# Kernel optimization log

Measured on AMD Instinct MI355X. Metric: run time of the kernel, lower is better.

## Reference

```python
import jax, jax.numpy as jnp
import numpy as np

B, N, E = 2, 20000, 320000
ND, ED, HD, L = 64, 32, 256, 4


def setup_inputs() -> dict:
    key = jax.random.key(0)
    ks = jax.random.split(key, 16)
    w = lambda k, shape: jax.random.normal(k, shape, jnp.float32) / np.sqrt(shape[-2])
    return {
        "node_features": jax.random.normal(ks[0], (B, N, ND), jnp.float32),
        "edge_indices": jax.random.randint(ks[1], (B, E, 2), 0, N, jnp.int64),
        "edge_features": jax.random.normal(ks[2], (B, E, ED), jnp.float32),
        "in_W": w(ks[3], (ND, HD)),
        "in_b": jnp.zeros((HD,), jnp.float32),
        "mW1": w(ks[4], (L, 2 * HD + ED, HD)),
        "mb1": jnp.zeros((L, HD), jnp.float32),
        "mW2": w(ks[5], (L, HD, HD)),
        "mb2": jnp.zeros((L, HD), jnp.float32),
        "uW1": w(ks[6], (L, HD + HD, HD)),
        "ub1": jnp.zeros((L, HD), jnp.float32),
        "uW2": w(ks[7], (L, HD, HD)),
        "ub2": jnp.zeros((L, HD), jnp.float32),
        "out_W": w(ks[8], (HD, ND)),
        "out_b": jnp.zeros((ND,), jnp.float32),
    }


def _mp_layer(h, edge_indices, edge_features, W1, b1, W2, b2, V1, c1, V2, c2):
    """One message passing layer, vmapped over batch of graphs."""
    def per_graph(nodes, edges, efeat):
        src = nodes[edges[:, 0]]                      # [E, HD] gather
        dst = nodes[edges[:, 1]]                      # [E, HD] gather
        msg_in = jnp.concatenate([src, dst, efeat], axis=-1)  # [E, 2HD+ED]
        msg = jax.nn.gelu(msg_in @ W1 + b1) @ W2 + b2          # [E, HD]
        agg = jnp.zeros((nodes.shape[0], W2.shape[1]), nodes.dtype)
        agg = agg.at[edges[:, 1]].add(msg)                     # scatter-add [N, HD]
        upd_in = jnp.concatenate([nodes, agg], axis=-1)        # [N, 2HD]
        return jax.nn.gelu(upd_in @ V1 + c1) @ V2 + c2         # [N, HD]

    return jax.vmap(per_graph)(h, edge_indices, edge_features)


def reference(node_features, edge_indices, edge_features, in_W, in_b,
              mW1, mb1, mW2, mb2, uW1, ub1, uW2, ub2, out_W, out_b):
    h = node_features @ in_W + in_b                  # [B, N, HD]
    num_layers = mW1.shape[0]
    for l in range(num_layers):
        h_new = _mp_layer(h, edge_indices, edge_features,
                          mW1[l], mb1[l], mW2[l], mb2[l],
                          uW1[l], ub1[l], uW2[l], ub2[l])
        h = h + h_new                                # residual
    return h @ out_W + out_b                         # [B, N, ND]
```

## Files before the change

### kernel.cpp

```cpp
#include <hip/hip_runtime.h>

#define NN 20000
#define NE 320000
#define NB 2
#define HDIM 256
#define NDIM 64
#define EDIM 32
#define NL 4
#define CHUNK 16

typedef short short8 __attribute__((ext_vector_type(8)));
typedef float f32x4 __attribute__((ext_vector_type(4)));

__device__ __forceinline__ float gelu_af(float x) {
    float x3 = x * x * x;
    float e = exp2f(2.3022082f * fmaf(0.044715f, x3, x));
    return fmaf(-x, __builtin_amdgcn_rcpf(e + 1.0f), x);
}

__device__ __forceinline__ unsigned short f2bf(float f) {
    unsigned int x = __float_as_uint(f);
    unsigned int r = (x + 0x7fffu + ((x >> 16) & 1u)) >> 16;
    return (unsigned short)r;
}
__device__ __forceinline__ float bf2f(unsigned short h) {
    return __uint_as_float(((unsigned int)h) << 16);
}

__global__ __launch_bounds__(256) void tr_k(
    const float* __restrict__ inW, const float* __restrict__ mW1,
    const float* __restrict__ mW2, const float* __restrict__ uW1,
    const float* __restrict__ uW2, const float* __restrict__ outW,
    unsigned short* __restrict__ dst)
{
    const int id = blockIdx.z;
    const float* src; int K, N; size_t doff;
    if (id == 0)       { src = inW;  K = 64;  N = 256; doff = 0; }
    else if (id <= 4)  { int l = id - 1;  src = mW1 + (size_t)l * 544 * 256; K = 544; N = 256; doff = 16384   + (size_t)l * 139264; }
    else if (id <= 8)  { int l = id - 5;  src = mW2 + (size_t)l * 256 * 256; K = 256; N = 256; doff = 573440  + (size_t)l * 65536;  }
    else if (id <= 12) { int l = id - 9;  src = uW1 + (size_t)l * 512 * 256; K = 512; N = 256; doff = 835584  + (size_t)l * 131072; }
    else if (id <= 16) { int l = id - 13; src = uW2 + (size_t)l * 256 * 256; K = 256; N = 256; doff = 1359872 + (size_t)l * 65536;  }
    else               { src = outW; K = 256; N = 64;  doff = 1622016; }

    const int k0 = blockIdx.x * 32, n0 = blockIdx.y * 32;
    if (k0 >= K || n0 >= N) return;

    __shared__ float tile[32][33];
    const int tx = threadIdx.x & 31, ty = threadIdx.x >> 5;
    #pragma unroll
    for (int i = 0; i < 4; ++i) {
        int k = k0 + ty + i * 8, n = n0 + tx;
        tile[ty + i * 8][tx] = (k < K && n < N) ? src[(size_t)k * N + n] : 0.f;
    }
    __syncthreads();
    #pragma unroll
    for (int i = 0; i < 4; ++i) {
        int n = n0 + ty + i * 8, k = k0 + tx;
        if (n < N && k < K) dst[doff + (size_t)n * K + k] = f2bf(tile[tx][ty + i * 8]);
    }
}

__global__ __launch_bounds__(256) void wv_k(
    const float* __restrict__ mW2, const float* __restrict__ uW1,
    unsigned short* __restrict__ w2v1bT)
{
    const int l = blockIdx.z;
    const float* W2  = mW2 + (size_t)l * 65536;
    const float* V1b = uW1 + (size_t)l * 131072 + 65536;
    const int n0 = blockIdx.x * 16, k0 = blockIdx.y * 16;
    const int tx = threadIdx.x & 15, ty = threadIdx.x >> 4;
    __shared__ float sW[16][17], sV[16][17];
    float acc = 0.f;
    for (int j0 = 0; j0 < 256; j0 += 16) {
        sW[ty][tx] = W2[(size_t)(k0 + ty) * 256 + j0 + tx];
        sV[ty][tx] = V1b[(size_t)(j0 + ty) * 256 + n0 + tx];
        __syncthreads();
        #pragma unroll
        for (int jj = 0; jj < 16; ++jj)
            acc = fmaf(sW[ty][jj], sV[jj][tx], acc);
        __syncthreads();
    }
    w2v1bT[(size_t)l * 65536 + (size_t)(n0 + tx) * 256 + (k0 + ty)] = f2bf(acc);
}

__global__ void bv_k(const float* __restrict__ mb1, const float* __restrict__ mb2,
                     const float* __restrict__ uW1,
                     float* __restrict__ b2v, float* __restrict__ bias512)
{
    const int l = blockIdx.x, t = threadIdx.x;
    if (t < 256) {
        const float* V1b = uW1 + (size_t)l * 131072 + 65536;
        const float* b2  = mb2 + l * 256;
        float s = 0.f;
        for (int j = 0; j < 256; ++j) s = fmaf(b2[j], V1b[(size_t)j * 256 + t], s);
        b2v[l * 256 + t] = s;
    }
    bias512[l * 512 + t] = (t < 256) ? 0.f : mb1[l * 256 + (t - 256)];
}

template <int MODE, int ASPLIT, int CSPLIT>
__global__ __launch_bounds__(256) void mgemm_k(
    const float* __restrict__ A,
    const unsigned short* __restrict__ Ah, const unsigned short* __restrict__ Al,
    const unsigned short* __restrict__ BT, int ldb,
    const unsigned short* __restrict__ A2h, const unsigned short* __restrict__ A2l,
    const unsigned short* __restrict__ BT2, int ldb2,
    const float* __restrict__ bias, const float* __restrict__ bias2,
    const float* __restrict__ degf,
    float* __restrict__ C, unsigned short* __restrict__ Ch, unsigned short* __restrict__ Cl,
    int M, int N, int K, int K2, int bkoff)
{
    __shared__ unsigned char smem[64 * 80 * 2 + 128 * 80];
    unsigned char* ahi = smem;
    unsigned char* alo = smem + 64 * 80;
    unsigned char* btl = smem + 64 * 80 * 2;

    const int tid = threadIdx.x;
    const int bm = blockIdx.x * 64;
    const int bn = blockIdx.y * 128;
    const int w = tid >> 6, lane = tid & 63;
    const int wr = w >> 1, wc = w & 1;
    const int lrow = lane & 15, lg = lane >> 4;

    f32x4 acc[2][4];
    #pragma unroll
    for (int i = 0; i < 2; ++i)
        #pragma unroll
        for (int j = 0; j < 4; ++j) acc[i][j] = (f32x4){0.f, 0.f, 0.f, 0.f};

    const int t1 = K >> 5, t2 = K2 >> 5;
    for (int t = 0; t < t1 + t2; ++t) {
        int k0, lda, ldbv;
        const float* Ap; const unsigned short* Ahp; const unsigned short* Alp;
        const unsigned short* Bp;
        if (t < t1) { Ap = A;  Ahp = Ah;  Alp = Al;  Bp = BT;  k0 = t * 32;        lda = K;  ldbv = ldb;  }
        else        { Ap = nullptr; Ahp = A2h; Alp = A2l; Bp = BT2; k0 = (t - t1) * 32; lda = K2; ldbv = ldb2; }

        {
            const int row = tid >> 2, kq = (tid & 3) * 8;
            const int m = bm + row;
            if (ASPLIT == 1) {
                uint4 hv = make_uint4(0u, 0u, 0u, 0u), lv = hv;
                if (m < M) {
                    hv = *(const uint4*)&Ahp[(size_t)m * lda + k0 + kq];
                    lv = *(const uint4*)&Alp[(size_t)m * lda + k0 + kq];
                }
                *(uint4*)(ahi + row * 80 + kq * 2) = hv;
                *(uint4*)(alo + row * 80 + kq * 2) = lv;
            } else if (ASPLIT == 2) {
                uint4 hv = make_uint4(0u, 0u, 0u, 0u);
                if (m < M) hv = *(const uint4*)&Ahp[(size_t)m * lda + k0 + kq];
                *(uint4*)(ahi + row * 80 + kq * 2) = hv;
            } else {
                float4 v0 = make_float4(0.f, 0.f, 0.f, 0.f), v1 = v0;
                if (m < M) {
                    v0 = *(const float4*)&Ap[(size_t)m * lda + k0 + kq];
                    v1 = *(const float4*)&Ap[(size_t)m * lda + k0 + kq + 4];
                }
                float vv[8] = {v0.x, v0.y, v0.z, v0.w, v1.x, v1.y, v1.z, v1.w};
                unsigned short hh[8], ll[8];
                #pragma unroll
                for (int j = 0; j < 8; ++j) {
                    hh[j] = f2bf(vv[j]);
                    ll[j] = f2bf(vv[j] - bf2f(hh[j]));
                }
                ushort4 ph0 = {hh[0], hh[1], hh[2], hh[3]}, ph1 = {hh[4], hh[5], hh[6], hh[7]};
                ushort4 pl0 = {ll[0], ll[1], ll[2], ll[3]}, pl1 = {ll[4], ll[5], ll[6], ll[7]};
                *(ushort4*)(ahi + row * 80 + kq * 2)     = ph0;
                *(ushort4*)(ahi + row * 80 + kq * 2 + 8) = ph1;
                *(ushort4*)(alo + row * 80 + kq * 2)     = pl0;
                *(ushort4*)(alo + row * 80 + kq * 2 + 8) = pl1;
            }
        }
        {
            const int row = tid >> 1, half = tid & 1;
            const int n = bn + row;
            const unsigned short* brow = Bp + (size_t)(n & 255) * ldbv + (n >> 8) * bkoff;
            #pragma unroll
            for (int c = 0; c < 2; ++c) {
                const int q = half * 2 + c;
                uint4 d = make_uint4(0u, 0u, 0u, 0u);
                if (n < N) d = *(const uint4*)&brow[k0 + q * 8];
                *(uint4*)(btl + row * 80 + q * 16) = d;
            }
        }
        __syncthreads();

        short8 ah[2], al[2], bfr[4];
        #pragma unroll
        for (int mi = 0; mi < 2; ++mi) {
            const int r = wr * 32 + mi * 16 + lrow;
            ah[mi] = *(const short8*)(ahi + r * 80 + lg * 16);
            if (ASPLIT != 2) al[mi] = *(const short8*)(alo + r * 80 + lg * 16);
        }
        #pragma unroll
        for (int ni = 0; ni < 4; ++ni) {
            const int r = wc * 64 + ni * 16 + lrow;
            bfr[ni] = *(const short8*)(btl + r * 80 + lg * 16);
        }
        #pragma unroll
        for (int mi = 0; mi < 2; ++mi)
            #pragma unroll
            for (int ni = 0; ni < 4; ++ni) {
                acc[mi][ni] = __builtin_amdgcn_mfma_f32_16x16x32_bf16(ah[mi], bfr[ni], acc[mi][ni], 0, 0, 0);
                if (ASPLIT != 2)
                    acc[mi][ni] = __builtin_amdgcn_mfma_f32_16x16x32_bf16(al[mi], bfr[ni], acc[mi][ni], 0, 0, 0);
            }
        __syncthreads();
    }

    #pragma unroll
    for (int mi = 0; mi < 2; ++mi) {
        #pragma unroll
        for (int ni = 0; ni < 4; ++ni) {
            const int ncol = bn + wc * 64 + ni * 16 + lrow;
            if (ncol >= N) continue;
            const float bv = bias ? bias[ncol] : 0.f;
            const float b2vv = (MODE == 4) ? bias2[ncol] : 0.f;
            const int mbase = bm + wr * 32 + mi * 16 + lg * 4;
            #pragma unroll
            for (int r = 0; r < 4; ++r) {
                const int m = mbase + r;
                if (m >= M) continue;
                const size_t cb = (size_t)m * N + ncol;
                float v = acc[mi][ni][r];
                if (MODE == 0)      v += bv;
                else if (MODE == 3) v += bf2f(Ch[cb]) + bf2f(Cl[cb]) + bv;
                else                v = gelu_af(v + degf[m] * b2vv + bv);
                if (CSPLIT == 1) {
                    unsigned short hi = f2bf(v);
                    unsigned short lo = f2bf(v - bf2f(hi));
                    Ch[cb] = hi; Cl[cb] = lo;
                } else if (CSPLIT == 2) {
                    Ch[cb] = f2bf(v);
                } else {
                    C[cb] = v;
                }
            }
        }
    }
}

__global__ void hist2_k(const int* __restrict__ ei, int* __restrict__ cnt) {
    int i = blockIdx.x * blockDim.x + threadIdx.x;
    if (i < NB * NE) {
        const int g = i / NE, e = i - g * NE;
        atomicAdd(&cnt[g * NN + ei[(size_t)g * NE * 2 + 2 * e + 1]], 1);
    }
}

__global__ void scan2_k(const int* __restrict__ cnt_all, int* __restrict__ row_ptr_all,
                        int* __restrict__ cursor_all, float* __restrict__ degf_all) {
    const int g = blockIdx.x;
    const int* cnt = cnt_all + g * NN;
    int* row_ptr = row_ptr_all + g * (NN + 1);
    int* cursor  = cursor_all + g * NN;
    float* degf  = degf_all + g * NN;
    __shared__ int part[256];
    int tid = threadIdx.x;
    const int per = (NN + 255) >> 8;
    int s0 = tid * per;
    int s1 = s0 + per; if (s1 > NN) s1 = NN; if (s0 > NN) s0 = NN;
    int sum = 0;
    for (int i = s0; i < s1; ++i) sum += cnt[i];
    part[tid] = sum;
    __syncthreads();
    if (tid == 0) {
        int r = 0;
        for (int i = 0; i < 256; ++i) { int v = part[i]; part[i] = r; r += v; }
    }
    __syncthreads();
    int off = part[tid];
    for (int i = s0; i < s1; ++i) {
        int c = cnt[i];
        row_ptr[i] = off; cursor[i] = off; degf[i] = (float)c;
        off += c;
    }
    if (tid == 255) row_ptr[NN] = off;
}

__global__ void fill2_k(const int* __restrict__ ei, int* __restrict__ cursor,
                        int2* __restrict__ csr_pack) {
    int i = blockIdx.x * blockDim.x + threadIdx.x;
    if (i < NB * NE) {
        const int g = i / NE, e = i - g * NE;
        const int* eig = ei + (size_t)g * NE * 2;
        int s = eig[2 * e + 0];
        int d = eig[2 * e + 1];
        int pos = atomicAdd(&cursor[g * NN + d], 1);
        csr_pack[(size_t)g * NE + pos] = make_int2(s, e);
    }
}

__global__ __launch_bounds__(128) void edge_agg9_k(
    const unsigned short* __restrict__ T12b,
    const float* __restrict__ efeat,
    const unsigned short* __restrict__ w1t,
    const int2* __restrict__ csr_pack, const int* __restrict__ row_ptr,
    unsigned short* __restrict__ Shi)
{
    __shared__ unsigned short efo[2][CHUNK * 260];

    const int tid = threadIdx.x;
    const int g   = blockIdx.x / (NN / 2);
    const int blk = blockIdx.x % (NN / 2);
    const int wave = tid >> 6, lane = tid & 63;
    const int lrow = lane & 15, lg = lane >> 4;
    const int d = blk * 2 + wave;

    const unsigned short* T12g = T12b + (size_t)g * NN * 512;
    const float* efg  = efeat + (size_t)g * NE * EDIM;
    const int2* cpG   = csr_pack + (size_t)g * NE;
    const int* rpG    = row_ptr + (size_t)g * (NN + 1);

    const int dstart = rpG[d], dend = rpG[d + 1];
    const int c0 = lane * 4;
    const char* tb = (const char*)T12g;

    short8 bfrag[16];
    #pragma unroll
    for (int ni = 0; ni < 16; ++ni)
        bfrag[ni] = *(const short8*)&w1t[(size_t)(ni * 16 + lrow) * 544 + 512 + lg * 8];

    const ushort4 hdu = *(const ushort4*)(tb + (unsigned)d * 1024u + 512u + (unsigned)c0 * 2u);
    const float4 hd = make_float4(bf2f(hdu.x), bf2f(hdu.y), bf2f(hdu.z), bf2f(hdu.w));
    float4 acc = make_float4(0.f, 0.f, 0.f, 0.f);
    unsigned short* efw = &efo[wave][0];

    for (int P = dstart; P < dend; P += CHUNK) {
        const int nv = dend - P < CHUNK ? dend - P : CHUNK;
        int pos = P + lrow; if (pos >= dend) pos = dend - 1;

        const int2 cp = cpG[pos];
        const int myid = cp.x, eid = cp.y;

        const float* er = &efg[(size_t)eid * EDIM + lg * 8];
        float4 v0 = *(const float4*)er;
        float4 v1 = *(const float4*)(er + 4);
        short8 af;
        af[0] = (short)f2bf(v0.x); af[1] = (short)f2bf(v0.y);
        af[2] = (short)f2bf(v0.z); af[3] = (short)f2bf(v0.w);
        af[4] = (short)f2bf(v1.x); af[5] = (short)f2bf(v1.y);
        af[6] = (short)f2bf(v1.z); af[7] = (short)f2bf(v1.w);

        #pragma unroll
        for (int ni = 0; ni < 16; ++ni) {
            f32x4 a4 = (f32x4){0.f, 0.f, 0.f, 0.f};
            a4 = __builtin_amdgcn_mfma_f32_16x16x32_bf16(af, bfrag[ni], a4, 0, 0, 0);
            #pragma unroll
            for (int r = 0; r < 4; ++r)
                efw[(4 * lg + r) * 260 + ni * 16 + lrow] = f2bf(a4[r]);
        }

        for (int p = P; p < P + nv; p += 4) {
            const int nc = P + nv - p;
            int sj[4]; ushort4 hsu[4]; ushort4 ef4[4];
            #pragma unroll
            for (int j = 0; j < 4; ++j) {
                const int q = p + ((j < nc) ? j : 0);
                sj[j] = __shfl(myid, q - P, 64);
            }
            #pragma unroll
            for (int j = 0; j < 4; ++j) {
                const int q = p + ((j < nc) ? j : 0);
                hsu[j] = *(const ushort4*)(tb + (unsigned)sj[j] * 1024u + (unsigned)c0 * 2u);
                ef4[j] = *(const ushort4*)&efw[(q - P) * 260 + c0];
            }
            #pragma unroll
            for (int j = 0; j < 4; ++j) {
                if (j < nc) {
                    acc.x += gelu_af(bf2f(hsu[j].x) + hd.x + bf2f(ef4[j].x));
                    acc.y += gelu_af(bf2f(hsu[j].y) + hd.y + bf2f(ef4[j].y));
                    acc.z += gelu_af(bf2f(hsu[j].z) + hd.z + bf2f(ef4[j].z));
                    acc.w += gelu_af(bf2f(hsu[j].w) + hd.w + bf2f(ef4[j].w));
                }
            }
        }
    }

    ushort4 ho;
    ho.x = f2bf(acc.x); ho.y = f2bf(acc.y);
    ho.z = f2bf(acc.z); ho.w = f2bf(acc.w);
    *(ushort4*)&Shi[((size_t)g * NN + d) * HDIM + c0] = ho;
}

extern "C" void kernel_launch(void* const* d_in, const int* in_sizes, int n_in,
                              void* d_out, int out_size, void* d_ws, size_t ws_size,
                              hipStream_t stream)
{
    const float* nf    = (const float*)d_in[0];
    const int*   ei    = (const int*)  d_in[1];
    const float* efeat = (const float*)d_in[2];
    const float* inW   = (const float*)d_in[3];
    const float* inb   = (const float*)d_in[4];
    const float* mW1   = (const float*)d_in[5];
    const float* mb1   = (const float*)d_in[6];
    const float* mW2   = (const float*)d_in[7];
    const float* mb2   = (const float*)d_in[8];
    const float* uW1   = (const float*)d_in[9];
    const float* ub1   = (const float*)d_in[10];
    const float* uW2   = (const float*)d_in[11];
    const float* ub2   = (const float*)d_in[12];
    const float* outW  = (const float*)d_in[13];
    const float* outb  = (const float*)d_in[14];
    float* outp = (float*)d_out;

    const int MT = NB * NN;

    char* p = (char*)d_ws;
    auto carve = [&](size_t bytes) -> void* {
        void* r = (void*)p;
        p += (bytes + 255) & ~(size_t)255;
        return r;
    };
    unsigned short* hS  = (unsigned short*)carve((size_t)2 * MT * HDIM * 2);
    unsigned short* T3S = (unsigned short*)carve((size_t)MT * HDIM * 2);
    unsigned short* T12b = (unsigned short*)carve((size_t)MT * 512 * 2);
    unsigned short* US = T12b;
    int2* csr_pack = (int2*)carve((size_t)NB * NE * 8);
    int* row_ptr = (int*)carve((size_t)NB * (NN + 1) * 4);
    int* cursor  = (int*)carve((size_t)NB * NN * 4);
    int* cnt     = (int*)carve((size_t)NB * NN * 4);
    float* degf  = (float*)carve((size_t)MT * 4);
    unsigned short* wtbuf  = (unsigned short*)carve((size_t)1638400 * 2);
    unsigned short* w2v1bT = (unsigned short*)carve((size_t)4 * 65536 * 2);
    float* b2v     = (float*)carve((size_t)4 * 256 * 4);
    float* bias512 = (float*)carve((size_t)4 * 512 * 4);
    (void)ws_size; (void)in_sizes; (void)n_in; (void)out_size;

    unsigned short* hHi  = hS;   unsigned short* hLo  = hS  + (size_t)MT * HDIM;
    unsigned short* t3S  = T3S;
    unsigned short* uS   = US;

    const dim3 blk(256);
    const dim3 gIn(625, 2), gHsHd(625, 4), gU(625, 2), gRes(625, 2), gOut(625, 1);
    const dim3 gE(NB * NN / 2);
    const dim3 blkE(128);

    tr_k<<<dim3(17, 8, 18), blk, 0, stream>>>(inW, mW1, mW2, uW1, uW2, outW, wtbuf);
    wv_k<<<dim3(16, 16, 4), blk, 0, stream>>>(mW2, uW1, w2v1bT);
    bv_k<<<dim3(4), dim3(512), 0, stream>>>(mb1, mb2, uW1, b2v, bias512);

    const unsigned short* wtIn  = wtbuf;
    const unsigned short* wtW1  = wtbuf + 16384;
    const unsigned short* wtU1  = wtbuf + 835584;
    const unsigned short* wtU2  = wtbuf + 1359872;
    const unsigned short* wtOut = wtbuf + 1622016;

    hipMemsetAsync(cnt, 0, (size_t)NB * NN * sizeof(int), stream);
    hist2_k<<<(NB * NE + 255) / 256, blk, 0, stream>>>(ei, cnt);
    scan2_k<<<dim3(NB), blk, 0, stream>>>(cnt, row_ptr, cursor, degf);
    fill2_k<<<(NB * NE + 255) / 256, blk, 0, stream>>>(ei, cursor, csr_pack);

    mgemm_k<0, 0, 1><<<gIn, blk, 0, stream>>>(
        nf, nullptr, nullptr, wtIn, NDIM,
        nullptr, nullptr, nullptr, 0,
        inb, nullptr, nullptr,
        nullptr, hHi, hLo, MT, HDIM, NDIM, 0, 0);

    for (int l = 0; l < NL; ++l) {
        const unsigned short* w1t = wtW1 + (size_t)l * 139264;
        const unsigned short* u1t = wtU1 + (size_t)l * 131072;
        const unsigned short* u2t = wtU2 + (size_t)l * 65536;

        mgemm_k<0, 2, 2><<<gHsHd, blk, 0, stream>>>(
            nullptr, hHi, nullptr, w1t, 544,
            nullptr, nullptr, nullptr, 0,
            bias512 + l * 512, nullptr, nullptr,
            nullptr, T12b, nullptr, MT, 512, HDIM, 0, 256);

        edge_agg9_k<<<gE, blkE, 0, stream>>>(T12b, efeat, w1t,
                                             csr_pack, row_ptr, t3S);

        mgemm_k<4, 2, 2><<<gU, blk, 0, stream>>>(
            nullptr, hHi, nullptr, u1t, 512,
            t3S, nullptr, w2v1bT + (size_t)l * 65536, 256,
            ub1 + l * HDIM, b2v + l * 256, degf,
            nullptr, uS, nullptr, MT, HDIM, HDIM, HDIM, 0);

        mgemm_k<3, 2, 1><<<gRes, blk, 0, stream>>>(
            nullptr, uS, nullptr, u2t, HDIM,
            nullptr, nullptr, nullptr, 0,
            ub2 + l * HDIM, nullptr, nullptr,
            nullptr, hHi, hLo, MT, HDIM, HDIM, 0, 0);
    }

    mgemm_k<0, 1, 0><<<gOut, blk, 0, stream>>>(
        nullptr, hHi, hLo, wtOut, HDIM,
        nullptr, nullptr, nullptr, 0,
        outb, nullptr, nullptr,
        outp, nullptr, nullptr, MT, NDIM, HDIM, 0, 0);
}
```

Baseline: 1.120 ms.

## Use 128x128 tiles for bf16 layer GEMMs and one-wave edge aggregation blocks

Splits the GEMM kernel in two. The bf16-only layer GEMMs (hs/hd, update, residual) move to a new kernel with 128x128 block tiles, so each wave computes a 64x64 sub-tile for more MFMA work per LDS load. The split-precision GEMMs for the input and output projections keep the old 64x128 kernel. The edge aggregation kernel changes from two waves per 128-thread block to one wave per 64-thread block, which doubles the block count and halves the shared memory per block. The larger GEMM tile raises register pressure and cuts the grid to 313 row blocks, which may lower occupancy.

```diff
diff --git a/kernel.cpp b/kernel.cpp
--- a/kernel.cpp
+++ b/kernel.cpp
@@ -103,12 +103,9 @@
     const float* __restrict__ A,
     const unsigned short* __restrict__ Ah, const unsigned short* __restrict__ Al,
     const unsigned short* __restrict__ BT, int ldb,
-    const unsigned short* __restrict__ A2h, const unsigned short* __restrict__ A2l,
-    const unsigned short* __restrict__ BT2, int ldb2,
-    const float* __restrict__ bias, const float* __restrict__ bias2,
-    const float* __restrict__ degf,
+    const float* __restrict__ bias,
     float* __restrict__ C, unsigned short* __restrict__ Ch, unsigned short* __restrict__ Cl,
-    int M, int N, int K, int K2, int bkoff)
+    int M, int N, int K)
 {
     __shared__ unsigned char smem[64 * 80 * 2 + 128 * 80];
     unsigned char* ahi = smem;
@@ -128,34 +125,25 @@
         #pragma unroll
         for (int j = 0; j < 4; ++j) acc[i][j] = (f32x4){0.f, 0.f, 0.f, 0.f};
 
-    const int t1 = K >> 5, t2 = K2 >> 5;
-    for (int t = 0; t < t1 + t2; ++t) {
-        int k0, lda, ldbv;
-        const float* Ap; const unsigned short* Ahp; const unsigned short* Alp;
-        const unsigned short* Bp;
-        if (t < t1) { Ap = A;  Ahp = Ah;  Alp = Al;  Bp = BT;  k0 = t * 32;        lda = K;  ldbv = ldb;  }
-        else        { Ap = nullptr; Ahp = A2h; Alp = A2l; Bp = BT2; k0 = (t - t1) * 32; lda = K2; ldbv = ldb2; }
-
+    const int t1 = K >> 5;
+    for (int t = 0; t < t1; ++t) {
+        const int k0 = t * 32;
         {
             const int row = tid >> 2, kq = (tid & 3) * 8;
             const int m = bm + row;
             if (ASPLIT == 1) {
                 uint4 hv = make_uint4(0u, 0u, 0u, 0u), lv = hv;
                 if (m < M) {
-                    hv = *(const uint4*)&Ahp[(size_t)m * lda + k0 + kq];
-                    lv = *(const uint4*)&Alp[(size_t)m * lda + k0 + kq];
+                    hv = *(const uint4*)&Ah[(size_t)m * K + k0 + kq];
+                    lv = *(const uint4*)&Al[(size_t)m * K + k0 + kq];
                 }
                 *(uint4*)(ahi + row * 80 + kq * 2) = hv;
                 *(uint4*)(alo + row * 80 + kq * 2) = lv;
-            } else if (ASPLIT == 2) {
-                uint4 hv = make_uint4(0u, 0u, 0u, 0u);
-                if (m < M) hv = *(const uint4*)&Ahp[(size_t)m * lda + k0 + kq];
-                *(uint4*)(ahi + row * 80 + kq * 2) = hv;
             } else {
                 float4 v0 = make_float4(0.f, 0.f, 0.f, 0.f), v1 = v0;
                 if (m < M) {
-                    v0 = *(const float4*)&Ap[(size_t)m * lda + k0 + kq];
-                    v1 = *(const float4*)&Ap[(size_t)m * lda + k0 + kq + 4];
+                    v0 = *(const float4*)&A[(size_t)m * K + k0 + kq];
+                    v1 = *(const float4*)&A[(size_t)m * K + k0 + kq + 4];
                 }
                 float vv[8] = {v0.x, v0.y, v0.z, v0.w, v1.x, v1.y, v1.z, v1.w};
                 unsigned short hh[8], ll[8];
@@ -175,12 +163,11 @@
         {
             const int row = tid >> 1, half = tid & 1;
             const int n = bn + row;
-            const unsigned short* brow = Bp + (size_t)(n & 255) * ldbv + (n >> 8) * bkoff;
             #pragma unroll
             for (int c = 0; c < 2; ++c) {
                 const int q = half * 2 + c;
                 uint4 d = make_uint4(0u, 0u, 0u, 0u);
-                if (n < N) d = *(const uint4*)&brow[k0 + q * 8];
+                if (n < N) d = *(const uint4*)&BT[(size_t)n * ldb + k0 + q * 8];
                 *(uint4*)(btl + row * 80 + q * 16) = d;
             }
         }
@@ -191,7 +178,7 @@
         for (int mi = 0; mi < 2; ++mi) {
             const int r = wr * 32 + mi * 16 + lrow;
             ah[mi] = *(const short8*)(ahi + r * 80 + lg * 16);
-            if (ASPLIT != 2) al[mi] = *(const short8*)(alo + r * 80 + lg * 16);
+            al[mi] = *(const short8*)(alo + r * 80 + lg * 16);
         }
         #pragma unroll
         for (int ni = 0; ni < 4; ++ni) {
@@ -203,21 +190,119 @@
             #pragma unroll
             for (int ni = 0; ni < 4; ++ni) {
                 acc[mi][ni] = __builtin_amdgcn_mfma_f32_16x16x32_bf16(ah[mi], bfr[ni], acc[mi][ni], 0, 0, 0);
-                if (ASPLIT != 2)
-                    acc[mi][ni] = __builtin_amdgcn_mfma_f32_16x16x32_bf16(al[mi], bfr[ni], acc[mi][ni], 0, 0, 0);
+                acc[mi][ni] = __builtin_amdgcn_mfma_f32_16x16x32_bf16(al[mi], bfr[ni], acc[mi][ni], 0, 0, 0);
             }
         __syncthreads();
     }
 
     #pragma unroll
     for (int mi = 0; mi < 2; ++mi) {
+        #pragma unroll
+        for (int ni = 0; ni < 4; ++ni) {
+            const int ncol = bn + wc * 64 + ni * 16 + lrow;
+            if (ncol >= N) continue;
+            const float bv = bias ? bias[ncol] : 0.f;
+            const int mbase = bm + wr * 32 + mi * 16 + lg * 4;
+            #pragma unroll
+            for (int r = 0; r < 4; ++r) {
+                const int m = mbase + r;
+                if (m >= M) continue;
+                const size_t cb = (size_t)m * N + ncol;
+                float v = acc[mi][ni][r] + bv;
+                if (CSPLIT == 1) {
+                    unsigned short hi = f2bf(v);
+                    unsigned short lo = f2bf(v - bf2f(hi));
+                    Ch[cb] = hi; Cl[cb] = lo;
+                } else {
+                    C[cb] = v;
+                }
+            }
+        }
+    }
+}
+
+template <int MODE, int CSPLIT>
+__global__ __launch_bounds__(256) void mgemm2_k(
+    const unsigned short* __restrict__ Ah, const unsigned short* __restrict__ BT, int ldb,
+    const unsigned short* __restrict__ A2h, const unsigned short* __restrict__ BT2, int ldb2,
+    const float* __restrict__ bias, const float* __restrict__ bias2,
+    const float* __restrict__ degf,
+    unsigned short* __restrict__ Ch, unsigned short* __restrict__ Cl,
+    int M, int N, int K, int K2, int bkoff)
+{
+    __shared__ unsigned char smem[128 * 80 * 2];
+    unsigned char* abuf = smem;
+    unsigned char* bbuf = smem + 128 * 80;
+
+    const int tid = threadIdx.x;
+    const int bm = blockIdx.x * 128;
+    const int bn = blockIdx.y * 128;
+    const int w = tid >> 6, lane = tid & 63;
+    const int wr = w >> 1, wc = w & 1;
+    const int lrow = lane & 15, lg = lane >> 4;
+
+    f32x4 acc[4][4];
+    #pragma unroll
+    for (int i = 0; i < 4; ++i)
+        #pragma unroll
+        for (int j = 0; j < 4; ++j) acc[i][j] = (f32x4){0.f, 0.f, 0.f, 0.f};
+
+    const int t1 = K >> 5, t2 = K2 >> 5;
+    for (int t = 0; t < t1 + t2; ++t) {
+        int k0, lda, ldbv;
+        const unsigned short* Ap; const unsigned short* Bp;
+        if (t < t1) { Ap = Ah;  Bp = BT;  k0 = t * 32;        lda = K;  ldbv = ldb;  }
+        else        { Ap = A2h; Bp = BT2; k0 = (t - t1) * 32; lda = K2; ldbv = ldb2; }
+
+        {
+            const int row = tid >> 1, sg = (tid & 1) * 16;
+            const int m = bm + row;
+            uint4 d0 = make_uint4(0u, 0u, 0u, 0u), d1 = d0;
+            if (m < M) {
+                d0 = *(const uint4*)&Ap[(size_t)m * lda + k0 + sg];
+                d1 = *(const uint4*)&Ap[(size_t)m * lda + k0 + sg + 8];
+            }
+            *(uint4*)(abuf + row * 80 + sg * 2)      = d0;
+            *(uint4*)(abuf + row * 80 + sg * 2 + 16) = d1;
+        }
+        {
+            const int row = tid >> 1, sg = (tid & 1) * 16;
+            const int n = bn + row;
+            const unsigned short* brow = Bp + (size_t)(n & 255) * ldbv + (n >> 8) * bkoff;
+            uint4 d0 = make_uint4(0u, 0u, 0u, 0u), d1 = d0;
+            if (n < N) {
+                d0 = *(const uint4*)&brow[k0 + sg];
+                d1 = *(const uint4*)&brow[k0 + sg + 8];
+            }
+            *(uint4*)(bbuf + row * 80 + sg * 2)      = d0;
+            *(uint4*)(bbuf + row * 80 + sg * 2 + 16) = d1;
+        }
+        __syncthreads();
+
+        short8 ah[4], bfr[4];
+        #pragma unroll
+        for (int mi = 0; mi < 4; ++mi)
+            ah[mi] = *(const short8*)(abuf + (wr * 64 + mi * 16 + lrow) * 80 + lg * 16);
+        #pragma unroll
+        for (int ni = 0; ni < 4; ++ni)
+            bfr[ni] = *(const short8*)(bbuf + (wc * 64 + ni * 16 + lrow) * 80 + lg * 16);
+        #pragma unroll
+        for (int mi = 0; mi < 4; ++mi)
+            #pragma unroll
+            for (int ni = 0; ni < 4; ++ni)
+                acc[mi][ni] = __builtin_amdgcn_mfma_f32_16x16x32_bf16(ah[mi], bfr[ni], acc[mi][ni], 0, 0, 0);
+        __syncthreads();
+    }
+
+    #pragma unroll
+    for (int mi = 0; mi < 4; ++mi) {
         #pragma unroll
         for (int ni = 0; ni < 4; ++ni) {
             const int ncol = bn + wc * 64 + ni * 16 + lrow;
             if (ncol >= N) continue;
             const float bv = bias ? bias[ncol] : 0.f;
             const float b2vv = (MODE == 4) ? bias2[ncol] : 0.f;
-            const int mbase = bm + wr * 32 + mi * 16 + lg * 4;
+            const int mbase = bm + wr * 64 + mi * 16 + lg * 4;
             #pragma unroll
             for (int r = 0; r < 4; ++r) {
                 const int m = mbase + r;
@@ -231,10 +316,8 @@
                     unsigned short hi = f2bf(v);
                     unsigned short lo = f2bf(v - bf2f(hi));
                     Ch[cb] = hi; Cl[cb] = lo;
-                } else if (CSPLIT == 2) {
+                } else {
                     Ch[cb] = f2bf(v);
-                } else {
-                    C[cb] = v;
                 }
             }
         }
@@ -292,21 +375,19 @@
     }
 }
 
-__global__ __launch_bounds__(128) void edge_agg9_k(
+__global__ __launch_bounds__(64) void edge_agg10_k(
     const unsigned short* __restrict__ T12b,
     const float* __restrict__ efeat,
     const unsigned short* __restrict__ w1t,
     const int2* __restrict__ csr_pack, const int* __restrict__ row_ptr,
     unsigned short* __restrict__ Shi)
 {
-    __shared__ unsigned short efo[2][CHUNK * 260];
-
-    const int tid = threadIdx.x;
-    const int g   = blockIdx.x / (NN / 2);
-    const int blk = blockIdx.x % (NN / 2);
-    const int wave = tid >> 6, lane = tid & 63;
+    __shared__ unsigned short efo[CHUNK * 260];
+
+    const int g   = blockIdx.x / NN;
+    const int d   = blockIdx.x % NN;
+    const int lane = threadIdx.x & 63;
     const int lrow = lane & 15, lg = lane >> 4;
-    const int d = blk * 2 + wave;
 
     const unsigned short* T12g = T12b + (size_t)g * NN * 512;
     const float* efg  = efeat + (size_t)g * NE * EDIM;
@@ -325,7 +406,6 @@
     const ushort4 hdu = *(const ushort4*)(tb + (unsigned)d * 1024u + 512u + (unsigned)c0 * 2u);
     const float4 hd = make_float4(bf2f(hdu.x), bf2f(hdu.y), bf2f(hdu.z), bf2f(hdu.w));
     float4 acc = make_float4(0.f, 0.f, 0.f, 0.f);
-    unsigned short* efw = &efo[wave][0];
 
     for (int P = dstart; P < dend; P += CHUNK) {
         const int nv = dend - P < CHUNK ? dend - P : CHUNK;
@@ -349,7 +429,7 @@
             a4 = __builtin_amdgcn_mfma_f32_16x16x32_bf16(af, bfrag[ni], a4, 0, 0, 0);
             #pragma unroll
             for (int r = 0; r < 4; ++r)
-                efw[(4 * lg + r) * 260 + ni * 16 + lrow] = f2bf(a4[r]);
+                efo[(4 * lg + r) * 260 + ni * 16 + lrow] = f2bf(a4[r]);
         }
 
         for (int p = P; p < P + nv; p += 4) {
@@ -364,7 +444,7 @@
             for (int j = 0; j < 4; ++j) {
                 const int q = p + ((j < nc) ? j : 0);
                 hsu[j] = *(const ushort4*)(tb + (unsigned)sj[j] * 1024u + (unsigned)c0 * 2u);
-                ef4[j] = *(const ushort4*)&efw[(q - P) * 260 + c0];
+                ef4[j] = *(const ushort4*)&efo[(q - P) * 260 + c0];
             }
             #pragma unroll
             for (int j = 0; j < 4; ++j) {
@@ -433,9 +513,10 @@
     unsigned short* uS   = US;
 
     const dim3 blk(256);
-    const dim3 gIn(625, 2), gHsHd(625, 4), gU(625, 2), gRes(625, 2), gOut(625, 1);
-    const dim3 gE(NB * NN / 2);
-    const dim3 blkE(128);
+    const dim3 gIn(625, 2), gOut(625, 1);
+    const dim3 gHsHd(313, 4), gU(313, 2), gRes(313, 2);
+    const dim3 gE(NB * NN);
+    const dim3 blkE(64);
 
     tr_k<<<dim3(17, 8, 18), blk, 0, stream>>>(inW, mW1, mW2, uW1, uW2, outW, wtbuf);
     wv_k<<<dim3(16, 16, 4), blk, 0, stream>>>(mW2, uW1, w2v1bT);
@@ -454,40 +535,36 @@
 
     mgemm_k<0, 0, 1><<<gIn, blk, 0, stream>>>(
         nf, nullptr, nullptr, wtIn, NDIM,
-        nullptr, nullptr, nullptr, 0,
-        inb, nullptr, nullptr,
-        nullptr, hHi, hLo, MT, HDIM, NDIM, 0, 0);
+        inb, nullptr, hHi, hLo, MT, HDIM, NDIM);
 
     for (int l = 0; l < NL; ++l) {
         const unsigned short* w1t = wtW1 + (size_t)l * 139264;
         const unsigned short* u1t = wtU1 + (size_t)l * 131072;
         const unsigned short* u2t = wtU2 + (size_t)l * 65536;
 
-        mgemm_k<0, 2, 2><<<gHsHd, blk, 0, stream>>>(
-            nullptr, hHi, nullptr, w1t, 544,
-            nullptr, nullptr, nullptr, 0,
+        mgemm2_k<0, 2><<<gHsHd, blk, 0, stream>>>(
+            hHi, w1t, 544,
+            nullptr, nullptr, 0,
             bias512 + l * 512, nullptr, nullptr,
-            nullptr, T12b, nullptr, MT, 512, HDIM, 0, 256);
-
-        edge_agg9_k<<<gE, blkE, 0, stream>>>(T12b, efeat, w1t,
-                                             csr_pack, row_ptr, t3S);
-
-        mgemm_k<4, 2, 2><<<gU, blk, 0, stream>>>(
-            nullptr, hHi, nullptr, u1t, 512,
-            t3S, nullptr, w2v1bT + (size_t)l * 65536, 256,
+            T12b, nullptr, MT, 512, HDIM, 0, 256);
+
+        edge_agg10_k<<<gE, blkE, 0, stream>>>(T12b, efeat, w1t,
+                                              csr_pack, row_ptr, t3S);
+
+        mgemm2_k<4, 2><<<gU, blk, 0, stream>>>(
+            hHi, u1t, 512,
+            t3S, w2v1bT + (size_t)l * 65536, 256,
             ub1 + l * HDIM, b2v + l * 256, degf,
-            nullptr, uS, nullptr, MT, HDIM, HDIM, HDIM, 0);
-
-        mgemm_k<3, 2, 1><<<gRes, blk, 0, stream>>>(
-            nullptr, uS, nullptr, u2t, HDIM,
-            nullptr, nullptr, nullptr, 0,
+            uS, nullptr, MT, HDIM, HDIM, HDIM, 0);
+
+        mgemm2_k<3, 1><<<gRes, blk, 0, stream>>>(
+            uS, u2t, HDIM,
+            nullptr, nullptr, 0,
             ub2 + l * HDIM, nullptr, nullptr,
-            nullptr, hHi, hLo, MT, HDIM, HDIM, 0, 0);
+            hHi, hLo, MT, HDIM, HDIM, 0, 0);
     }
 
     mgemm_k<0, 1, 0><<<gOut, blk, 0, stream>>>(
         nullptr, hHi, hLo, wtOut, HDIM,
-        nullptr, nullptr, nullptr, 0,
-        outb, nullptr, nullptr,
-        outp, nullptr, nullptr, MT, NDIM, HDIM, 0, 0);
-}
+        outb, outp, nullptr, nullptr, MT, NDIM, HDIM);
+}
```

Measured after the change: 1.257 ms. +12.3%, slower.
